# Performance work log

Hardware: AMD Instinct MI355X
Metric: run time of the kernel (lower is better)

Reference implementation:

```python
import jax, jax.numpy as jnp
import numpy as np

N_NODES = 50000
N_EDGES = 800000
IN_CH = 16
OUT_CH = 16
HID = 32


def setup_inputs() -> dict:
    key = jax.random.key(0)
    ks = jax.random.split(key, 10)
    features = jax.random.normal(ks[0], (N_NODES, IN_CH), dtype=jnp.float32)
    coords = jax.random.normal(ks[1], (N_NODES, 3), dtype=jnp.float32)
    # edges without self-loops (avoids zero-distance edges)
    row = jax.random.randint(ks[2], (N_EDGES,), 0, N_NODES, dtype=jnp.int32)
    off = jax.random.randint(ks[3], (N_EDGES,), 1, N_NODES, dtype=jnp.int32)
    col = (row + off) % N_NODES
    edge_index = jnp.stack([row, col], axis=0)
    # params (fan-in scaled like torch defaults, roughly)
    w1 = jax.random.normal(ks[4], (1, HID), dtype=jnp.float32)
    b1 = jnp.zeros((HID,), dtype=jnp.float32)
    w2 = jax.random.normal(ks[5], (HID, HID), dtype=jnp.float32) / np.sqrt(HID)
    b2 = jnp.zeros((HID,), dtype=jnp.float32)
    wc = jax.random.normal(ks[6], (HID, IN_CH * OUT_CH), dtype=jnp.float32) / np.sqrt(HID)
    bc = jnp.zeros((IN_CH * OUT_CH,), dtype=jnp.float32)
    return {"features": features, "coords": coords, "edge_index": edge_index,
            "w1": w1, "b1": b1, "w2": w2, "b2": b2, "wc": wc, "bc": bc}


def reference(features, coords, edge_index, w1, b1, w2, b2, wc, bc):
    row, col = edge_index[0], edge_index[1]
    rel_pos = coords[row] - coords[col]                      # [E, 3]
    distances = jnp.sqrt(jnp.sum(rel_pos * rel_pos, axis=-1, keepdims=True))  # [E, 1]
    h = jax.nn.silu(distances @ w1 + b1)                     # [E, H]
    h = jax.nn.silu(h @ w2 + b2)                             # [E, H]
    coeffs = (h @ wc + bc).reshape(-1, OUT_CH, IN_CH)        # [E, out, in]
    # Faithful to torch einsum 'noi,ei->no': the edge axes of coeffs and
    # neighbor_features are DISTINCT labels, so features[col] is summed over
    # all edges, then contracted with each edge's coeff matrix.
    feat_sum = jnp.sum(features[col], axis=0)                # [in]
    messages = jnp.einsum('eoi,i->eo', coeffs, feat_sum)     # [E, out]
    out = jnp.zeros((features.shape[0], OUT_CH), dtype=features.dtype)
    out = out.at[row].add(messages)                          # scatter-add
    return out
```

## Files before the change

### kernel.cpp

```cpp
#include <hip/hip_runtime.h>
#include <hip/hip_bf16.h>

#define IN_CH 16
#define OUT_CH 16
#define HID 32
#define NSLICE 8
#define SDEG 16
#define G_TAB 8192
#define DMAX 16.0f
#define R1_BLOCKS 64
#define TB 256

__device__ __forceinline__ float silu(float x) {
  return x * __frcp_rn(1.f + __expf(-x));
}

__global__ __launch_bounds__(256) void k_zero(int4* __restrict__ p, int n4) {
  int i = blockIdx.x * blockDim.x + threadIdx.x;
  if (i < n4) p[i] = make_int4(0, 0, 0, 0);
}

__global__ __launch_bounds__(256) void k_pass1(
    const float* __restrict__ feat, const float* __restrict__ coords,
    const int* __restrict__ row, const int* __restrict__ col, int E, int N,
    int* __restrict__ cnt8, float* __restrict__ bucket,
    float* __restrict__ partials) {
  int e = blockIdx.x * blockDim.x + threadIdx.x;
  int lane = threadIdx.x & 63;
  int wave = threadIdx.x >> 6;
  bool act = (e < E);

  float s[IN_CH];
#pragma unroll
  for (int i = 0; i < IN_CH; ++i) s[i] = 0.f;

  int r = 0, pos = SDEG;
  float d = 0.f;
  int slice = blockIdx.x & (NSLICE - 1);

  if (act) {
    r = row[e];
    int c = col[e];

    float rx = coords[r * 3 + 0] - coords[c * 3 + 0];
    float ry = coords[r * 3 + 1] - coords[c * 3 + 1];
    float rz = coords[r * 3 + 2] - coords[c * 3 + 2];
    d = sqrtf(rx * rx + ry * ry + rz * rz);

    pos = atomicAdd(&cnt8[r * NSLICE + slice], 1);

    const float4* fp = reinterpret_cast<const float4*>(feat + (size_t)c * IN_CH);
    float4 a = fp[0], b = fp[1], cc = fp[2], dd = fp[3];
    s[0] = a.x;  s[1] = a.y;  s[2] = a.z;  s[3] = a.w;
    s[4] = b.x;  s[5] = b.y;  s[6] = b.z;  s[7] = b.w;
    s[8] = cc.x; s[9] = cc.y; s[10] = cc.z; s[11] = cc.w;
    s[12] = dd.x; s[13] = dd.y; s[14] = dd.z; s[15] = dd.w;
  }

  __shared__ float red[4][IN_CH];
#pragma unroll
  for (int i = 0; i < IN_CH; ++i) {
    float v = s[i];
#pragma unroll
    for (int off = 32; off > 0; off >>= 1) v += __shfl_down(v, off);
    s[i] = v;
  }
  if (lane == 0) {
#pragma unroll
    for (int i = 0; i < IN_CH; ++i) red[wave][i] = s[i];
  }
  __syncthreads();
  if (threadIdx.x < IN_CH) {
    int i = threadIdx.x;
    partials[(size_t)blockIdx.x * IN_CH + i] =
        red[0][i] + red[1][i] + red[2][i] + red[3][i];
  }

  if (act && pos < SDEG)
    bucket[(size_t)r * (NSLICE * SDEG) + slice * SDEG + pos] = d;
}

__global__ __launch_bounds__(256) void k_reduce1(
    const float* __restrict__ partials, int nrows, float* __restrict__ stage2) {
  __shared__ float red[16][IN_CH];
  int t = threadIdx.x;
  int ch = t & 15, g = t >> 4;
  int stream_id = blockIdx.x * 16 + g;
  int stride = 16 * gridDim.x;
  float a = 0.f;
  for (int rr = stream_id; rr < nrows; rr += stride)
    a += partials[(size_t)rr * IN_CH + ch];
  red[g][ch] = a;
  __syncthreads();
  if (t < IN_CH) {
    float s = 0.f;
#pragma unroll
    for (int g2 = 0; g2 < 16; ++g2) s += red[g2][t];
    stage2[(size_t)blockIdx.x * IN_CH + t] = s;
  }
}

__global__ __launch_bounds__(512) void k_wce(
    const float* __restrict__ rows_in, int nrows,
    const float* __restrict__ wc, const float* __restrict__ bc,
    float* __restrict__ wce, float* __restrict__ bce) {
  __shared__ float seg[32][IN_CH];
  __shared__ float sfs[IN_CH];
  int t = threadIdx.x;
  {
    int ch = t & 15, sg = t >> 4;
    float a = 0.f;
    for (int rr = sg; rr < nrows; rr += 32)
      a += rows_in[(size_t)rr * IN_CH + ch];
    seg[sg][ch] = a;
  }
  __syncthreads();
  if (t < IN_CH) {
    float a = 0.f;
#pragma unroll
    for (int sg = 0; sg < 32; ++sg) a += seg[sg][t];
    sfs[t] = a;
  }
  __syncthreads();

  int k = t >> 4, o = t & 15;
  float acc = 0.f;
#pragma unroll
  for (int i = 0; i < IN_CH; ++i)
    acc += wc[k * (IN_CH * OUT_CH) + o * IN_CH + i] * sfs[i];
  wce[t] = acc;

  if (t < OUT_CH) {
    float a = 0.f;
#pragma unroll
    for (int i = 0; i < IN_CH; ++i) a += bc[t * IN_CH + i] * sfs[i];
    bce[t] = a;
  }
}

__global__ __launch_bounds__(TB) void k_table(
    const float* __restrict__ w1, const float* __restrict__ b1,
    const float* __restrict__ w2, const float* __restrict__ b2,
    const float* __restrict__ wce, const float* __restrict__ bce,
    float* __restrict__ tableP) {
  __shared__ float F[TB][OUT_CH];
  int base = blockIdx.x * (TB - 1);
  int i = base + threadIdx.x;

  float m[OUT_CH];
#pragma unroll
  for (int o = 0; o < OUT_CH; ++o) m[o] = 0.f;

  if (i < G_TAB) {
    float d = (float)i * (DMAX / (float)(G_TAB - 1));

    float h1[HID];
#pragma unroll
    for (int k = 0; k < HID; ++k) h1[k] = silu(d * w1[k] + b1[k]);

    float h2[HID];
#pragma unroll
    for (int k = 0; k < HID; ++k) h2[k] = b2[k];
#pragma unroll
    for (int k = 0; k < HID; ++k) {
      float hk = h1[k];
#pragma unroll
      for (int j = 0; j < HID; ++j) h2[j] += hk * w2[k * HID + j];
    }

#pragma unroll
    for (int o = 0; o < OUT_CH; ++o) m[o] = bce[o];
#pragma unroll
    for (int k = 0; k < HID; ++k) {
      float hk = silu(h2[k]);
#pragma unroll
      for (int o = 0; o < OUT_CH; ++o) m[o] += hk * wce[k * OUT_CH + o];
    }
  }

#pragma unroll
  for (int o = 0; o < OUT_CH; ++o) F[threadIdx.x][o] = m[o];
  __syncthreads();

  const int NV4 = (TB - 1) * OUT_CH * 2 / 4;
  for (int v = threadIdx.x; v < NV4; v += TB) {
    int flat = v * 4;
    int p = flat >> 5;
    int w = flat & 31;
    int c0 = w >> 1;
    int P = base + p;
    if (P < G_TAB - 1) {
      float4 val = make_float4(F[p][c0], F[p + 1][c0],
                               F[p][c0 + 1], F[p + 1][c0 + 1]);
      *reinterpret_cast<float4*>(tableP + ((size_t)P * OUT_CH + c0) * 2) = val;
    }
  }
}

__global__ __launch_bounds__(256) void k_gather_tab(
    const int* __restrict__ cnt8, const float* __restrict__ bucket, int N,
    const float* __restrict__ tableP, float* __restrict__ out) {
  int wave = threadIdx.x >> 6;
  int lane = threadIdx.x & 63;
  int n = blockIdx.x * 4 + wave;
  if (n >= N) return;

  int g = lane >> 4;
  int ch = lane & 15;

  const float2* bp =
      reinterpret_cast<const float2*>(bucket + (size_t)n * (NSLICE * SDEG));
  float2 d2 = bp[lane];

  int c8 = 0;
  if (lane < NSLICE) c8 = cnt8[n * NSLICE + lane];
  int cntA = min(__shfl(c8, g), SDEG);
  int cntB = min(__shfl(c8, g + 4), SDEG);

  int jmax = max(cntA, cntB);
#pragma unroll
  for (int off = 32; off > 0; off >>= 1)
    jmax = max(jmax, __shfl_xor(jmax, off));

  const float inv = (float)(G_TAB - 1) / DMAX;
  float acc = 0.f;
  for (int j = 0; j < jmax; ++j) {
    {
      int slot = g * SDEG + j;
      float dx = __shfl(d2.x, slot >> 1);
      float dy = __shfl(d2.y, slot >> 1);
      float d = (slot & 1) ? dy : dx;
      if (j < cntA) {
        float x = d * inv;
        int i0 = (int)x;
        i0 = min(i0, G_TAB - 2);
        float frac = x - (float)i0;
        float2 f = *reinterpret_cast<const float2*>(
            tableP + ((size_t)i0 * OUT_CH + ch) * 2);
        acc += f.x + frac * (f.y - f.x);
      }
    }
    {
      int slot = (g + 4) * SDEG + j;
      float dx = __shfl(d2.x, slot >> 1);
      float dy = __shfl(d2.y, slot >> 1);
      float d = (slot & 1) ? dy : dx;
      if (j < cntB) {
        float x = d * inv;
        int i0 = (int)x;
        i0 = min(i0, G_TAB - 2);
        float frac = x - (float)i0;
        float2 f = *reinterpret_cast<const float2*>(
            tableP + ((size_t)i0 * OUT_CH + ch) * 2);
        acc += f.x + frac * (f.y - f.x);
      }
    }
  }

  acc += __shfl_xor(acc, 16);
  acc += __shfl_xor(acc, 32);
  if (lane < OUT_CH) out[(size_t)n * OUT_CH + lane] = acc;
}

__global__ __launch_bounds__(256) void k_hist(
    const int* __restrict__ col, int E, int* __restrict__ ccnt) {
  int e = blockIdx.x * blockDim.x + threadIdx.x;
  if (e < E) atomicAdd(&ccnt[col[e]], 1);
}

__global__ __launch_bounds__(256) void k_fs(
    const float* __restrict__ feat, const int* __restrict__ ccnt, int N,
    float* __restrict__ partials) {
  int ch = threadIdx.x & 15;
  int slot = threadIdx.x >> 4;
  int gs = blockIdx.x * 16 + slot;
  int stride = 16 * gridDim.x;
  float a = 0.f;
  for (int n = gs; n < N; n += stride)
    a += (float)ccnt[n] * feat[(size_t)n * IN_CH + ch];
  __shared__ float red[16][IN_CH];
  red[slot][ch] = a;
  __syncthreads();
  if (threadIdx.x < IN_CH) {
    int i = threadIdx.x;
    float s = 0.f;
#pragma unroll
    for (int g = 0; g < 16; ++g) s += red[g][i];
    partials[(size_t)blockIdx.x * IN_CH + i] = s;
  }
}

__global__ __launch_bounds__(256) void k_edges_atomic(
    const float* __restrict__ coords, const int* __restrict__ row,
    const int* __restrict__ col, int E,
    const float* __restrict__ w1, const float* __restrict__ b1,
    const float* __restrict__ w2, const float* __restrict__ b2,
    const float* __restrict__ wce, const float* __restrict__ bce,
    float* __restrict__ out) {
  int e = blockIdx.x * blockDim.x + threadIdx.x;
  if (e >= E) return;
  int r = row[e], c = col[e];
  float rx = coords[r * 3 + 0] - coords[c * 3 + 0];
  float ry = coords[r * 3 + 1] - coords[c * 3 + 1];
  float rz = coords[r * 3 + 2] - coords[c * 3 + 2];
  float d = sqrtf(rx * rx + ry * ry + rz * rz);
  float h1[HID];
#pragma unroll
  for (int k = 0; k < HID; ++k) h1[k] = silu(d * w1[k] + b1[k]);
  float h2[HID];
#pragma unroll
  for (int k = 0; k < HID; ++k) h2[k] = b2[k];
#pragma unroll
  for (int k = 0; k < HID; ++k) {
    float hk = h1[k];
#pragma unroll
    for (int j = 0; j < HID; ++j) h2[j] += hk * w2[k * HID + j];
  }
  float m[OUT_CH];
#pragma unroll
  for (int o = 0; o < OUT_CH; ++o) m[o] = bce[o];
#pragma unroll
  for (int k = 0; k < HID; ++k) {
    float hk = silu(h2[k]);
#pragma unroll
    for (int o = 0; o < OUT_CH; ++o) m[o] += hk * wce[k * OUT_CH + o];
  }
  float* op = out + (size_t)r * OUT_CH;
#pragma unroll
  for (int o = 0; o < OUT_CH; ++o) atomicAdd(op + o, m[o]);
}

extern "C" void kernel_launch(void* const* d_in, const int* in_sizes, int n_in,
                              void* d_out, int out_size, void* d_ws,
                              size_t ws_size, hipStream_t stream) {
  const float* features = (const float*)d_in[0];
  const float* coords   = (const float*)d_in[1];
  const int*   eidx     = (const int*)d_in[2];
  const float* w1       = (const float*)d_in[3];
  const float* b1       = (const float*)d_in[4];
  const float* w2       = (const float*)d_in[5];
  const float* b2       = (const float*)d_in[6];
  const float* wc       = (const float*)d_in[7];
  const float* bc       = (const float*)d_in[8];

  const int E = in_sizes[2] / 2;
  const int N = in_sizes[0] / IN_CH;
  const int* row = eidx;
  const int* col = eidx + E;

  float* out = (float*)d_out;
  const int eb = (E + 255) / 256;

  float* wce      = (float*)d_ws;
  float* bce      = wce + 512;
  float* stage2   = bce + 16;
  float* partials = stage2 + R1_BLOCKS * IN_CH;
  float* tableP   = partials + (size_t)eb * IN_CH;
  int*   cnt8     = (int*)(tableP + (size_t)G_TAB * OUT_CH * 2);
  float* bucket   = (float*)(cnt8 + (size_t)N * NSLICE);

  size_t needed = (512 + 16 + (size_t)R1_BLOCKS * IN_CH + (size_t)eb * IN_CH +
                   (size_t)G_TAB * OUT_CH * 2) * 4 +
                  (size_t)N * NSLICE * 4 + (size_t)N * NSLICE * SDEG * 4;

  if (ws_size >= needed) {
    int n4 = (int)(((size_t)N * NSLICE) / 4);
    k_zero<<<(n4 + 255) / 256, 256, 0, stream>>>((int4*)cnt8, n4);
    k_pass1<<<eb, 256, 0, stream>>>(features, coords, row, col, E, N, cnt8,
                                    bucket, partials);
    k_reduce1<<<R1_BLOCKS, 256, 0, stream>>>(partials, eb, stage2);
    k_wce<<<1, 512, 0, stream>>>(stage2, R1_BLOCKS, wc, bc, wce, bce);
    int tb_grid = (G_TAB - 1 + (TB - 1) - 1) / (TB - 1) + 1;
    k_table<<<tb_grid, TB, 0, stream>>>(w1, b1, w2, b2, wce, bce, tableP);
    int gb = (N + 3) / 4;
    k_gather_tab<<<gb, 256, 0, stream>>>(cnt8, bucket, N, tableP, out);
  } else {
    float* partials_fb = bce + 16;
    int*   ccnt_fb     = (int*)(partials_fb + 64 * IN_CH);
    int nz4 = (N + 3) / 4;
    k_zero<<<(nz4 + 255) / 256, 256, 0, stream>>>((int4*)ccnt_fb, nz4);
    hipMemsetAsync(out, 0, (size_t)out_size * sizeof(float), stream);
    k_hist<<<eb, 256, 0, stream>>>(col, E, ccnt_fb);
    k_fs<<<64, 256, 0, stream>>>(features, ccnt_fb, N, partials_fb);
    k_wce<<<1, 512, 0, stream>>>(partials_fb, 64, wc, bc, wce, bce);
    k_edges_atomic<<<eb, 256, 0, stream>>>(coords, row, col, E, w1, b1, w2,
                                           b2, wce, bce, out);
  }
}
```

Measured before the change: 100.9 us.

## Pad slice counters, fuse reduction with wce, and regroup gather into four slices

Per-node slice counters are padded to 16 ints each, so counters for different (row, slice) pairs no longer share cache lines. The slice count drops from 8 to 4 with 32 slots per slice. The separate partial-reduction and wce kernels are merged into one kernel that uses a last-block-done atomic, which removes a launch. The gather loop now has each 16-lane group handle one slice and processes two distances per iteration with clamped indices. The trade-off is a counter array eight times larger to zero and a fence plus atomic at the end of the reduction.

```diff
diff --git a/kernel.cpp b/kernel.cpp
--- a/kernel.cpp
+++ b/kernel.cpp
@@ -4,11 +4,12 @@
 #define IN_CH 16
 #define OUT_CH 16
 #define HID 32
-#define NSLICE 8
-#define SDEG 16
+#define NSLICE 4
+#define SDEG 32
+#define CPAD 16
 #define G_TAB 8192
 #define DMAX 16.0f
-#define R1_BLOCKS 64
+#define RED_BLOCKS 64
 #define TB 256
 
 __device__ __forceinline__ float silu(float x) {
@@ -23,7 +24,7 @@
 __global__ __launch_bounds__(256) void k_pass1(
     const float* __restrict__ feat, const float* __restrict__ coords,
     const int* __restrict__ row, const int* __restrict__ col, int E, int N,
-    int* __restrict__ cnt8, float* __restrict__ bucket,
+    int* __restrict__ cnt_pad, float* __restrict__ bucket,
     float* __restrict__ partials) {
   int e = blockIdx.x * blockDim.x + threadIdx.x;
   int lane = threadIdx.x & 63;
@@ -47,7 +48,7 @@
     float rz = coords[r * 3 + 2] - coords[c * 3 + 2];
     d = sqrtf(rx * rx + ry * ry + rz * rz);
 
-    pos = atomicAdd(&cnt8[r * NSLICE + slice], 1);
+    pos = atomicAdd(&cnt_pad[((size_t)r * NSLICE + slice) * CPAD], 1);
 
     const float4* fp = reinterpret_cast<const float4*>(feat + (size_t)c * IN_CH);
     float4 a = fp[0], b = fp[1], cc = fp[2], dd = fp[3];
@@ -77,59 +78,66 @@
   }
 
   if (act && pos < SDEG)
-    bucket[(size_t)r * (NSLICE * SDEG) + slice * SDEG + pos] = d;
-}
-
-__global__ __launch_bounds__(256) void k_reduce1(
-    const float* __restrict__ partials, int nrows, float* __restrict__ stage2) {
+    bucket[((size_t)r * NSLICE + slice) * SDEG + pos] = d;
+}
+
+__global__ __launch_bounds__(256) void k_red(
+    const float* __restrict__ partials, int nrows,
+    const float* __restrict__ wc, const float* __restrict__ bc,
+    float* __restrict__ stage2, int* __restrict__ done,
+    float* __restrict__ wce, float* __restrict__ bce) {
   __shared__ float red[16][IN_CH];
+  __shared__ float sfs[IN_CH];
+  __shared__ int lastFlag;
   int t = threadIdx.x;
   int ch = t & 15, g = t >> 4;
-  int stream_id = blockIdx.x * 16 + g;
-  int stride = 16 * gridDim.x;
-  float a = 0.f;
-  for (int rr = stream_id; rr < nrows; rr += stride)
-    a += partials[(size_t)rr * IN_CH + ch];
-  red[g][ch] = a;
+
+  {
+    int stream_id = blockIdx.x * 16 + g;
+    int stride = 16 * RED_BLOCKS;
+    float a = 0.f;
+    for (int rr = stream_id; rr < nrows; rr += stride)
+      a += partials[(size_t)rr * IN_CH + ch];
+    red[g][ch] = a;
+  }
   __syncthreads();
   if (t < IN_CH) {
     float s = 0.f;
 #pragma unroll
     for (int g2 = 0; g2 < 16; ++g2) s += red[g2][t];
-    stage2[(size_t)blockIdx.x * IN_CH + t] = s;
-  }
-}
-
-__global__ __launch_bounds__(512) void k_wce(
-    const float* __restrict__ rows_in, int nrows,
-    const float* __restrict__ wc, const float* __restrict__ bc,
-    float* __restrict__ wce, float* __restrict__ bce) {
-  __shared__ float seg[32][IN_CH];
-  __shared__ float sfs[IN_CH];
-  int t = threadIdx.x;
+    stage2[blockIdx.x * IN_CH + t] = s;
+  }
+  __threadfence();
+  __syncthreads();
+  if (t == 0) lastFlag = (atomicAdd(done, 1) == RED_BLOCKS - 1);
+  __syncthreads();
+  if (!lastFlag) return;
+
+  __threadfence();
   {
-    int ch = t & 15, sg = t >> 4;
-    float a = 0.f;
-    for (int rr = sg; rr < nrows; rr += 32)
-      a += rows_in[(size_t)rr * IN_CH + ch];
-    seg[sg][ch] = a;
+    int sg = t >> 4;
+    float a = 0.f;
+    for (int rr = sg; rr < RED_BLOCKS; rr += 16)
+      a += stage2[rr * IN_CH + ch];
+    red[sg][ch] = a;
   }
   __syncthreads();
   if (t < IN_CH) {
-    float a = 0.f;
-#pragma unroll
-    for (int sg = 0; sg < 32; ++sg) a += seg[sg][t];
-    sfs[t] = a;
-  }
-  __syncthreads();
-
-  int k = t >> 4, o = t & 15;
-  float acc = 0.f;
-#pragma unroll
-  for (int i = 0; i < IN_CH; ++i)
-    acc += wc[k * (IN_CH * OUT_CH) + o * IN_CH + i] * sfs[i];
-  wce[t] = acc;
-
+    float s = 0.f;
+#pragma unroll
+    for (int g2 = 0; g2 < 16; ++g2) s += red[g2][t];
+    sfs[t] = s;
+  }
+  __syncthreads();
+
+  for (int idx = t; idx < HID * OUT_CH; idx += 256) {
+    int k = idx >> 4, o = idx & 15;
+    float acc = 0.f;
+#pragma unroll
+    for (int i = 0; i < IN_CH; ++i)
+      acc += wc[k * (IN_CH * OUT_CH) + o * IN_CH + i] * sfs[i];
+    wce[idx] = acc;
+  }
   if (t < OUT_CH) {
     float a = 0.f;
 #pragma unroll
@@ -198,7 +206,7 @@
 }
 
 __global__ __launch_bounds__(256) void k_gather_tab(
-    const int* __restrict__ cnt8, const float* __restrict__ bucket, int N,
+    const int* __restrict__ cnt_pad, const float* __restrict__ bucket, int N,
     const float* __restrict__ tableP, float* __restrict__ out) {
   int wave = threadIdx.x >> 6;
   int lane = threadIdx.x & 63;
@@ -212,54 +220,83 @@
       reinterpret_cast<const float2*>(bucket + (size_t)n * (NSLICE * SDEG));
   float2 d2 = bp[lane];
 
-  int c8 = 0;
-  if (lane < NSLICE) c8 = cnt8[n * NSLICE + lane];
-  int cntA = min(__shfl(c8, g), SDEG);
-  int cntB = min(__shfl(c8, g + 4), SDEG);
-
-  int jmax = max(cntA, cntB);
-#pragma unroll
-  for (int off = 32; off > 0; off >>= 1)
-    jmax = max(jmax, __shfl_xor(jmax, off));
+  int c = 0;
+  if (lane < NSLICE) c = cnt_pad[((size_t)n * NSLICE + lane) * CPAD];
+  int c0 = min(__shfl(c, 0), SDEG);
+  int c1 = min(__shfl(c, 1), SDEG);
+  int c2 = min(__shfl(c, 2), SDEG);
+  int c3 = min(__shfl(c, 3), SDEG);
+  int cntG = (g == 0) ? c0 : (g == 1) ? c1 : (g == 2) ? c2 : c3;
+  int jmax = max(max(c0, c1), max(c2, c3));
 
   const float inv = (float)(G_TAB - 1) / DMAX;
   float acc = 0.f;
-  for (int j = 0; j < jmax; ++j) {
-    {
-      int slot = g * SDEG + j;
-      float dx = __shfl(d2.x, slot >> 1);
-      float dy = __shfl(d2.y, slot >> 1);
-      float d = (slot & 1) ? dy : dx;
-      if (j < cntA) {
-        float x = d * inv;
-        int i0 = (int)x;
-        i0 = min(i0, G_TAB - 2);
-        float frac = x - (float)i0;
-        float2 f = *reinterpret_cast<const float2*>(
-            tableP + ((size_t)i0 * OUT_CH + ch) * 2);
-        acc += f.x + frac * (f.y - f.x);
-      }
+  for (int j = 0; j < jmax; j += 2) {
+    int half = (g * SDEG + j) >> 1;
+    float da = __shfl(d2.x, half);
+    float db = __shfl(d2.y, half);
+    bool pa = (j < cntG), pb = (j + 1 < cntG);
+
+    da = fminf(fmaxf(da, 0.f), DMAX);
+    db = fminf(fmaxf(db, 0.f), DMAX);
+    float xa = da * inv;
+    int ia = min((int)xa, G_TAB - 2);
+    float fa = xa - (float)ia;
+    float xb = db * inv;
+    int ib = min((int)xb, G_TAB - 2);
+    float fb = xb - (float)ib;
+
+    if (pa) {
+      float2 F = *reinterpret_cast<const float2*>(
+          tableP + ((size_t)ia * OUT_CH + ch) * 2);
+      acc += F.x + fa * (F.y - F.x);
     }
-    {
-      int slot = (g + 4) * SDEG + j;
-      float dx = __shfl(d2.x, slot >> 1);
-      float dy = __shfl(d2.y, slot >> 1);
-      float d = (slot & 1) ? dy : dx;
-      if (j < cntB) {
-        float x = d * inv;
-        int i0 = (int)x;
-        i0 = min(i0, G_TAB - 2);
-        float frac = x - (float)i0;
-        float2 f = *reinterpret_cast<const float2*>(
-            tableP + ((size_t)i0 * OUT_CH + ch) * 2);
-        acc += f.x + frac * (f.y - f.x);
-      }
+    if (pb) {
+      float2 F = *reinterpret_cast<const float2*>(
+          tableP + ((size_t)ib * OUT_CH + ch) * 2);
+      acc += F.x + fb * (F.y - F.x);
     }
   }
 
   acc += __shfl_xor(acc, 16);
   acc += __shfl_xor(acc, 32);
   if (lane < OUT_CH) out[(size_t)n * OUT_CH + lane] = acc;
+}
+
+__global__ __launch_bounds__(512) void k_wce_fb(
+    const float* __restrict__ rows_in, int nrows,
+    const float* __restrict__ wc, const float* __restrict__ bc,
+    float* __restrict__ wce, float* __restrict__ bce) {
+  __shared__ float seg[32][IN_CH];
+  __shared__ float sfs[IN_CH];
+  int t = threadIdx.x;
+  {
+    int ch = t & 15, sg = t >> 4;
+    float a = 0.f;
+    for (int rr = sg; rr < nrows; rr += 32)
+      a += rows_in[(size_t)rr * IN_CH + ch];
+    seg[sg][ch] = a;
+  }
+  __syncthreads();
+  if (t < IN_CH) {
+    float a = 0.f;
+#pragma unroll
+    for (int sg = 0; sg < 32; ++sg) a += seg[sg][t];
+    sfs[t] = a;
+  }
+  __syncthreads();
+  int k = t >> 4, o = t & 15;
+  float acc = 0.f;
+#pragma unroll
+  for (int i = 0; i < IN_CH; ++i)
+    acc += wc[k * (IN_CH * OUT_CH) + o * IN_CH + i] * sfs[i];
+  wce[t] = acc;
+  if (t < OUT_CH) {
+    float a = 0.f;
+#pragma unroll
+    for (int i = 0; i < IN_CH; ++i) a += bc[t * IN_CH + i] * sfs[i];
+    bce[t] = a;
+  }
 }
 
 __global__ __launch_bounds__(256) void k_hist(
@@ -349,41 +386,44 @@
   const int* col = eidx + E;
 
   float* out = (float*)d_out;
+  float* ws  = (float*)d_ws;
   const int eb = (E + 255) / 256;
 
-  float* wce      = (float*)d_ws;
-  float* bce      = wce + 512;
-  float* stage2   = bce + 16;
-  float* partials = stage2 + R1_BLOCKS * IN_CH;
-  float* tableP   = partials + (size_t)eb * IN_CH;
-  int*   cnt8     = (int*)(tableP + (size_t)G_TAB * OUT_CH * 2);
-  float* bucket   = (float*)(cnt8 + (size_t)N * NSLICE);
-
-  size_t needed = (512 + 16 + (size_t)R1_BLOCKS * IN_CH + (size_t)eb * IN_CH +
-                   (size_t)G_TAB * OUT_CH * 2) * 4 +
-                  (size_t)N * NSLICE * 4 + (size_t)N * NSLICE * SDEG * 4;
+  size_t off = 0;
+  float* wce = ws + off;      off += 512;
+  float* bce = ws + off;      off += 16;
+  float* stage2 = ws + off;   off += RED_BLOCKS * IN_CH;
+  float* partials = ws + off; off += (size_t)eb * IN_CH;
+  off = (off + 63) & ~(size_t)63;
+  float* tableP = ws + off;   off += (size_t)G_TAB * OUT_CH * 2;
+  off = (off + 63) & ~(size_t)63;
+  int* done = (int*)(ws + off);     off += 16;
+  int* cnt_pad = (int*)(ws + off);  off += (size_t)N * NSLICE * CPAD;
+  float* bucket = ws + off;         off += (size_t)N * NSLICE * SDEG;
+  size_t needed = off * 4;
 
   if (ws_size >= needed) {
-    int n4 = (int)(((size_t)N * NSLICE) / 4);
-    k_zero<<<(n4 + 255) / 256, 256, 0, stream>>>((int4*)cnt8, n4);
-    k_pass1<<<eb, 256, 0, stream>>>(features, coords, row, col, E, N, cnt8,
+    int n4 = (int)((16 + (size_t)N * NSLICE * CPAD) / 4);
+    k_zero<<<(n4 + 255) / 256, 256, 0, stream>>>((int4*)done, n4);
+    k_pass1<<<eb, 256, 0, stream>>>(features, coords, row, col, E, N, cnt_pad,
                                     bucket, partials);
-    k_reduce1<<<R1_BLOCKS, 256, 0, stream>>>(partials, eb, stage2);
-    k_wce<<<1, 512, 0, stream>>>(stage2, R1_BLOCKS, wc, bc, wce, bce);
+    k_red<<<RED_BLOCKS, 256, 0, stream>>>(partials, eb, wc, bc, stage2, done,
+                                          wce, bce);
     int tb_grid = (G_TAB - 1 + (TB - 1) - 1) / (TB - 1) + 1;
     k_table<<<tb_grid, TB, 0, stream>>>(w1, b1, w2, b2, wce, bce, tableP);
     int gb = (N + 3) / 4;
-    k_gather_tab<<<gb, 256, 0, stream>>>(cnt8, bucket, N, tableP, out);
+    k_gather_tab<<<gb, 256, 0, stream>>>(cnt_pad, bucket, N, tableP, out);
   } else {
     float* partials_fb = bce + 16;
     int*   ccnt_fb     = (int*)(partials_fb + 64 * IN_CH);
     int nz4 = (N + 3) / 4;
     k_zero<<<(nz4 + 255) / 256, 256, 0, stream>>>((int4*)ccnt_fb, nz4);
     hipMemsetAsync(out, 0, (size_t)out_size * sizeof(float), stream);
-    k_hist<<<eb, 256, 0, stream>>>(col, E, ccnt_fb);
+    k_hist<<<(E + 255) / 256, 256, 0, stream>>>(col, E, ccnt_fb);
     k_fs<<<64, 256, 0, stream>>>(features, ccnt_fb, N, partials_fb);
-    k_wce<<<1, 512, 0, stream>>>(partials_fb, 64, wc, bc, wce, bce);
-    k_edges_atomic<<<eb, 256, 0, stream>>>(coords, row, col, E, w1, b1, w2,
-                                           b2, wce, bce, out);
-  }
-}
+    k_wce_fb<<<1, 512, 0, stream>>>(partials_fb, 64, wc, bc, wce, bce);
+    k_edges_atomic<<<(E + 255) / 256, 256, 0, stream>>>(coords, row, col, E,
+                                                        w1, b1, w2, b2, wce,
+                                                        bce, out);
+  }
+}
```

Result: no change. 101.1 us (+0.2%).
